# Optimization experiments

Hardware: AMD Instinct MI355X
Metric: run time of the kernel (lower is better)

Reference implementation:

```python
import jax, jax.numpy as jnp
import numpy as np
import math

N_FREQ = 50
ENC_DIM = 4 * N_FREQ  # 200
D = 5
N_GENES = 1000
N_CELLS = 5000
N_FRAG = 200_000


def sine_encoding(coords):
    # frequencies: [f1,f1,f2,f2,...] length 2*N_FREQ; shifts: [0, pi/2, 0, pi/2, ...]
    i = jnp.arange(1, N_FREQ + 1, dtype=jnp.float32)
    freqs = jnp.repeat(1.0 / jnp.power(jnp.float32(1000.0), 2.0 * i / N_FREQ), 2)
    shifts = jnp.tile(jnp.array([0.0, math.pi / 2], jnp.float32), N_FREQ)
    # coords [F,2] -> [F,2,2*nf] -> [F,4*nf]
    return jnp.sin((coords[..., None] * freqs + shifts).reshape(coords.shape[0], -1))


def self_attention(x):
    # x: [G, i, D]; NOTE: scale uses sqrt(seq_len) = sqrt(x.shape[-2]) as in the original
    scores = jnp.einsum('gid,gjd->gij', x, x) / jnp.sqrt(jnp.float32(x.shape[1]))
    w = jax.nn.softmax(scores, axis=-1)
    return jnp.einsum('gij,gjd->gid', w, x)


def setup_inputs() -> dict:
    key = jax.random.key(0)
    ks = jax.random.split(key, 6)
    coordinates = jax.random.uniform(ks[0], (N_FRAG, 2), jnp.float32, -1000.0, 1000.0)
    genemapping = jax.random.randint(ks[1], (N_FRAG,), 0, N_GENES)
    local_cellxgene_ix = jax.random.randint(ks[2], (N_FRAG,), 0, N_CELLS * N_GENES)
    genes_oi = jnp.arange(N_GENES)
    # ragged groups: disjoint fragment index sets for group sizes 2, 3, 4
    n2 = jnp.arange(60000)             # 30000 pairs
    n3 = jnp.arange(60000) + 60000     # 20000 triples
    n4 = jnp.arange(60000) + 120000    # 15000 quads
    stdv = 1.0 / math.sqrt(D)
    weight1_frag = jax.random.uniform(ks[3], (N_GENES, ENC_DIM, D), jnp.float32, -stdv, stdv)
    weight1_expr = jnp.ones((N_GENES, D), jnp.float32)
    bias1 = jax.random.normal(ks[4], (N_GENES,), jnp.float32)  # mean_gene_expression
    return dict(coordinates=coordinates, genemapping=genemapping, n2=n2, n3=n3, n4=n4,
                local_cellxgene_ix=local_cellxgene_ix, genes_oi=genes_oi,
                weight1_frag=weight1_frag, weight1_expr=weight1_expr, bias1=bias1)


def reference(coordinates, genemapping, n2, n3, n4, local_cellxgene_ix, genes_oi,
              weight1_frag, weight1_expr, bias1):
    # FragmentEmbedder: sine encode, per-gene weight gather, contract, sigmoid
    enc = sine_encoding(coordinates)                                 # [F, 200]
    emb = jax.nn.sigmoid(jnp.einsum('fe,fed->fd', enc, weight1_frag[genemapping]))  # [F, 5]
    # ragged self-attention over fixed-size groups (2, 3, 4)
    for idx, i in ((n2, 2), (n3, 3), (n4, 4)):
        x = emb[idx].reshape(-1, i, D)
        emb = emb.at[idx].set(self_attention(x).reshape(-1, D))
    # EmbeddingGenePooler: segment sum over cell x gene
    pooled = jax.ops.segment_sum(emb, local_cellxgene_ix, num_segments=N_CELLS * N_GENES)
    cell_gene_embedding = pooled.reshape(N_CELLS, N_GENES, D)
    # EmbeddingToExpression: gene-wise weighted sum + mean expression bias
    return (cell_gene_embedding * weight1_expr[genes_oi]).sum(-1) + bias1[genes_oi]
```

## Files before the change

### kernel.cpp

```cpp
#include <hip/hip_runtime.h>
#include <math.h>

#define DD 5
#define NFREQ 50
#define NB 128

__global__ __launch_bounds__(256) void blockhist_kernel(
    const int* __restrict__ gm, int F, int chunk,
    int* __restrict__ bc, int n_genes, int* __restrict__ done) {
  __shared__ int cnt[1000];
  if (blockIdx.x == 0 && threadIdx.x == 0) *done = 0;
  for (int j = threadIdx.x; j < n_genes; j += blockDim.x) cnt[j] = 0;
  __syncthreads();
  int b = blockIdx.x;
  int lo = b * chunk;
  int hi = min(F, lo + chunk);
  for (int i = lo + threadIdx.x; i < hi; i += blockDim.x)
    atomicAdd(&cnt[gm[i]], 1);
  __syncthreads();
  for (int j = threadIdx.x; j < n_genes; j += blockDim.x)
    bc[j * NB + b] = cnt[j];
}

__global__ __launch_bounds__(256) void binscan_starts_kernel(
    int* __restrict__ bc, int n_genes, int* __restrict__ totals,
    int* __restrict__ starts, int* __restrict__ done, int nblocks) {
  __shared__ int s_amlast;
  __shared__ int s_ws[4];
  int lane = threadIdx.x & 63;
  int wv = threadIdx.x >> 6;
  int bin = blockIdx.x * 4 + wv;
  if (bin < n_genes) {
    int2* row = (int2*)(bc + (size_t)bin * NB);
    int2 v = row[lane];
    int p = v.x + v.y;
    int ip = p;
#pragma unroll
    for (int off = 1; off < 64; off <<= 1) {
      int q = __shfl_up(ip, off);
      if (lane >= off) ip += q;
    }
    int base = ip - p;
    int2 e;
    e.x = base;
    e.y = base + v.x;
    row[lane] = e;
    if (lane == 63) totals[bin] = ip;
  }
  __syncthreads();
  if (threadIdx.x == 0) {
    __threadfence();
    int tk = atomicAdd(done, 1);
    s_amlast = (tk == nblocks - 1);
  }
  __syncthreads();
  if (!s_amlast) return;
  __threadfence();
  int t = threadIdx.x;
  int4 v = make_int4(0, 0, 0, 0);
  if (4 * t < n_genes) v = ((const int4*)totals)[t];
  int p = v.x + v.y + v.z + v.w;
  int ip = p;
#pragma unroll
  for (int off = 1; off < 64; off <<= 1) {
    int q = __shfl_up(ip, off);
    if (lane >= off) ip += q;
  }
  if (lane == 63) s_ws[wv] = ip;
  __syncthreads();
  int add = 0;
#pragma unroll
  for (int i = 0; i < 4; ++i)
    if (i < wv) add += s_ws[i];
  int excl = add + ip - p;
  int4 e;
  e.x = excl;
  e.y = excl + v.x;
  e.z = e.y + v.y;
  e.w = e.z + v.z;
  if (4 * t < n_genes) ((int4*)starts)[t] = e;
  if (4 * t + 4 == n_genes) starts[n_genes] = e.w + v.w;
}

__global__ __launch_bounds__(256) void blockscatter_kernel(
    const int* __restrict__ gm, int F, int chunk,
    const int* __restrict__ bc, const int* __restrict__ starts,
    int* __restrict__ order, int n_genes) {
  __shared__ int cur[1000];
  int b = blockIdx.x;
  for (int j = threadIdx.x; j < n_genes; j += blockDim.x)
    cur[j] = starts[j] + bc[j * NB + b];
  __syncthreads();
  int lo = b * chunk;
  int hi = min(F, lo + chunk);
  for (int i = lo + threadIdx.x; i < hi; i += blockDim.x) {
    int g = gm[i];
    int p = atomicAdd(&cur[g], 1);
    order[p] = i;
  }
}

__global__ __launch_bounds__(256) void embed_kernel(
    const float2* __restrict__ coords, const int* __restrict__ order,
    const int* __restrict__ starts, const float* __restrict__ W,
    float* __restrict__ emb) {
  __shared__ float s_freq[NFREQ];
  if (threadIdx.x < NFREQ)
    s_freq[threadIdx.x] = exp2f(-0.39863137f * (float)(threadIdx.x + 1));
  __syncthreads();
  int g = blockIdx.x;
  int s0 = starts[g];
  int s1 = starts[g + 1];
  const float* __restrict__ Wg = W + (size_t)g * (4 * NFREQ * DD);

  for (int i = s0 + threadIdx.x; i < s1; i += blockDim.x) {
    int f = order[i];
    float2 xy = coords[f];
    float a0 = 0.f, a1 = 0.f, a2 = 0.f, a3 = 0.f, a4 = 0.f;
    for (int k = 0; k < NFREQ; ++k) {
      float fr = s_freq[k];
      float ax = xy.x * fr;
      float ay = xy.y * fr;
      float sx = __sinf(ax), cx = __cosf(ax);
      float sy = __sinf(ay), cy = __cosf(ay);
      const float* w0s = Wg + (2 * k) * DD;
      const float* w0c = w0s + DD;
      const float* w1s = Wg + (2 * NFREQ + 2 * k) * DD;
      const float* w1c = w1s + DD;
      a0 += sx * w0s[0] + cx * w0c[0] + sy * w1s[0] + cy * w1c[0];
      a1 += sx * w0s[1] + cx * w0c[1] + sy * w1s[1] + cy * w1c[1];
      a2 += sx * w0s[2] + cx * w0c[2] + sy * w1s[2] + cy * w1c[2];
      a3 += sx * w0s[3] + cx * w0c[3] + sy * w1s[3] + cy * w1c[3];
      a4 += sx * w0s[4] + cx * w0c[4] + sy * w1s[4] + cy * w1c[4];
    }
    float* e = emb + (size_t)f * DD;
    e[0] = 1.f / (1.f + __expf(-a0));
    e[1] = 1.f / (1.f + __expf(-a1));
    e[2] = 1.f / (1.f + __expf(-a2));
    e[3] = 1.f / (1.f + __expf(-a3));
    e[4] = 1.f / (1.f + __expf(-a4));
  }
}

template <int SZ>
__device__ __forceinline__ void attn_group(const int* __restrict__ idx,
                                           float* __restrict__ emb) {
  int fid[SZ];
  float x[SZ][DD];
#pragma unroll
  for (int a = 0; a < SZ; ++a) {
    fid[a] = idx[a];
    const float* p = emb + (size_t)fid[a] * DD;
#pragma unroll
    for (int d = 0; d < DD; ++d) x[a][d] = p[d];
  }
  const float scale = rsqrtf((float)SZ);
  float o[SZ][DD];
#pragma unroll
  for (int a = 0; a < SZ; ++a) {
    float sc[SZ];
    float m = -1e30f;
#pragma unroll
    for (int b = 0; b < SZ; ++b) {
      float dt = 0.f;
#pragma unroll
      for (int d = 0; d < DD; ++d) dt += x[a][d] * x[b][d];
      sc[b] = dt * scale;
      m = fmaxf(m, sc[b]);
    }
    float sum = 0.f;
#pragma unroll
    for (int b = 0; b < SZ; ++b) {
      sc[b] = __expf(sc[b] - m);
      sum += sc[b];
    }
    float inv = 1.f / sum;
#pragma unroll
    for (int d = 0; d < DD; ++d) {
      float acc = 0.f;
#pragma unroll
      for (int b = 0; b < SZ; ++b) acc += sc[b] * x[b][d];
      o[a][d] = acc * inv;
    }
  }
#pragma unroll
  for (int a = 0; a < SZ; ++a) {
    float* p = emb + (size_t)fid[a] * DD;
#pragma unroll
    for (int d = 0; d < DD; ++d) p[d] = o[a][d];
  }
}

__global__ __launch_bounds__(256) void attn_init_kernel(
    const int* __restrict__ n2, int g2,
    const int* __restrict__ n3, int g3,
    const int* __restrict__ n4, int g4,
    float* __restrict__ emb, float* __restrict__ out,
    const float* __restrict__ bias, const int* __restrict__ genes_oi,
    int n_genes, int total4) {
  int gtid = blockIdx.x * blockDim.x + threadIdx.x;
  int gs = gridDim.x * blockDim.x;
  int gtot = g2 + g3 + g4;
  for (int w = gtid; w < gtot; w += gs) {
    if (w < g2) attn_group<2>(n2 + (size_t)w * 2, emb);
    else if (w < g2 + g3) attn_group<3>(n3 + (size_t)(w - g2) * 3, emb);
    else attn_group<4>(n4 + (size_t)(w - g2 - g3) * 4, emb);
  }
  for (int v4 = gtid; v4 < total4; v4 += gs) {
    int idx = v4 * 4;
    int j = idx % n_genes;
    float4 vv;
    vv.x = bias[genes_oi[j + 0]];
    vv.y = bias[genes_oi[j + 1]];
    vv.z = bias[genes_oi[j + 2]];
    vv.w = bias[genes_oi[j + 3]];
    reinterpret_cast<float4*>(out)[v4] = vv;
  }
}

__global__ void pool_kernel(const float* __restrict__ emb, const int* __restrict__ lci,
                            const int* __restrict__ genes_oi,
                            const float* __restrict__ wexpr, int F, int n_genes,
                            float* __restrict__ out) {
  int t = blockIdx.x * blockDim.x + threadIdx.x;
  if (t >= F) return;
  int ix = lci[t];
  int gcol = ix % n_genes;
  int g = genes_oi[gcol];
  const float* e = emb + (size_t)t * DD;
  const float* w = wexpr + (size_t)g * DD;
  float s = e[0] * w[0] + e[1] * w[1] + e[2] * w[2] + e[3] * w[3] + e[4] * w[4];
  atomicAdd(out + ix, s);
}

extern "C" void kernel_launch(void* const* d_in, const int* in_sizes, int n_in,
                              void* d_out, int out_size, void* d_ws, size_t ws_size,
                              hipStream_t stream) {
  const float2* coords  = (const float2*)d_in[0];
  const int* gm         = (const int*)d_in[1];
  const int* n2         = (const int*)d_in[2];
  const int* n3         = (const int*)d_in[3];
  const int* n4         = (const int*)d_in[4];
  const int* lci        = (const int*)d_in[5];
  const int* genes_oi   = (const int*)d_in[6];
  const float* W        = (const float*)d_in[7];
  const float* wexpr    = (const float*)d_in[8];
  const float* bias     = (const float*)d_in[9];
  float* out            = (float*)d_out;

  const int F       = in_sizes[1];
  const int n_genes = in_sizes[6];
  const int g2 = in_sizes[2] / 2;
  const int g3 = in_sizes[3] / 3;
  const int g4 = in_sizes[4] / 4;

  char* ws = (char*)d_ws;
  size_t off = 0;
  float* emb   = (float*)(ws + off); off += (size_t)F * DD * sizeof(float);
  int* order   = (int*)(ws + off);   off += (size_t)F * sizeof(int);
  int* bc      = (int*)(ws + off);   off += (size_t)n_genes * NB * sizeof(int);
  off = (off + 15) & ~(size_t)15;
  int* starts  = (int*)(ws + off);   off += (size_t)(n_genes + 4) * sizeof(int);
  off = (off + 15) & ~(size_t)15;
  int* totals  = (int*)(ws + off);   off += (size_t)n_genes * sizeof(int);
  int* done    = (int*)(ws + off);   off += 4 * sizeof(int);

  const int tb = 256;
  const int chunk = (F + NB - 1) / NB;

  blockhist_kernel<<<NB, tb, 0, stream>>>(gm, F, chunk, bc, n_genes, done);
  int scan_blocks = (n_genes + 3) / 4;
  binscan_starts_kernel<<<scan_blocks, tb, 0, stream>>>(bc, n_genes, totals,
                                                        starts, done, scan_blocks);
  blockscatter_kernel<<<NB, tb, 0, stream>>>(gm, F, chunk, bc, starts, order, n_genes);
  embed_kernel<<<n_genes, tb, 0, stream>>>(coords, order, starts, W, emb);
  int total4 = out_size / 4;
  attn_init_kernel<<<1250, tb, 0, stream>>>(n2, g2, n3, g3, n4, g4,
                                            emb, out, bias, genes_oi,
                                            n_genes, total4);
  pool_kernel<<<(F + tb - 1) / tb, tb, 0, stream>>>(emb, lci, genes_oi, wexpr,
                                                    F, n_genes, out);
}
```

Before: 144.5 us.

## Fuse attention with pooling and move output bias init into histogram kernel

The attention step now feeds its outputs straight into the expression dot product and atomic pooling instead of writing emb back and reading it again in a separate pool kernel. A byte mask built during the scan kernel marks fragments that belong to groups, so the fused kernel pools only the ungrouped fragments directly. The bias initialisation of the large output moves into the first histogram kernel, which now runs with more blocks to overlap that fill with the histogram work. This removes one launch and a round trip of emb through memory, at the cost of clearing and scattering the mask and of scattered atomics issued from inside the attention loop.

```diff
diff --git a/kernel.cpp b/kernel.cpp
--- a/kernel.cpp
+++ b/kernel.cpp
@@ -5,28 +5,55 @@
 #define NFREQ 50
 #define NB 128
 
-__global__ __launch_bounds__(256) void blockhist_kernel(
+__global__ __launch_bounds__(256) void hist_init_kernel(
     const int* __restrict__ gm, int F, int chunk,
-    int* __restrict__ bc, int n_genes, int* __restrict__ done) {
+    int* __restrict__ bc, int n_genes, int* __restrict__ done,
+    unsigned char* __restrict__ mask,
+    float* __restrict__ out, const float* __restrict__ bias,
+    const int* __restrict__ genes_oi, int total4) {
   __shared__ int cnt[1000];
-  if (blockIdx.x == 0 && threadIdx.x == 0) *done = 0;
-  for (int j = threadIdx.x; j < n_genes; j += blockDim.x) cnt[j] = 0;
-  __syncthreads();
-  int b = blockIdx.x;
-  int lo = b * chunk;
-  int hi = min(F, lo + chunk);
-  for (int i = lo + threadIdx.x; i < hi; i += blockDim.x)
-    atomicAdd(&cnt[gm[i]], 1);
-  __syncthreads();
-  for (int j = threadIdx.x; j < n_genes; j += blockDim.x)
-    bc[j * NB + b] = cnt[j];
+  const int gtid = blockIdx.x * blockDim.x + threadIdx.x;
+  const int gs = gridDim.x * blockDim.x;
+  if (gtid == 0) *done = 0;
+  int F4 = F >> 2;
+  int* mask4 = (int*)mask;
+  for (int i = gtid; i < F4; i += gs) mask4[i] = 0;
+  for (int i = (F4 << 2) + gtid; i < F; i += gs) mask[i] = 0;
+  for (int v4 = gtid; v4 < total4; v4 += gs) {
+    int idx = v4 * 4;
+    int j = idx % n_genes;
+    float4 vv;
+    vv.x = bias[genes_oi[j + 0]];
+    vv.y = bias[genes_oi[j + 1]];
+    vv.z = bias[genes_oi[j + 2]];
+    vv.w = bias[genes_oi[j + 3]];
+    reinterpret_cast<float4*>(out)[v4] = vv;
+  }
+  if (blockIdx.x < NB) {
+    for (int j = threadIdx.x; j < n_genes; j += blockDim.x) cnt[j] = 0;
+    __syncthreads();
+    int b = blockIdx.x;
+    int lo = b * chunk;
+    int hi = min(F, lo + chunk);
+    for (int i = lo + threadIdx.x; i < hi; i += blockDim.x)
+      atomicAdd(&cnt[gm[i]], 1);
+    __syncthreads();
+    for (int j = threadIdx.x; j < n_genes; j += blockDim.x)
+      bc[j * NB + b] = cnt[j];
+  }
 }
 
 __global__ __launch_bounds__(256) void binscan_starts_kernel(
     int* __restrict__ bc, int n_genes, int* __restrict__ totals,
-    int* __restrict__ starts, int* __restrict__ done, int nblocks) {
+    int* __restrict__ starts, int* __restrict__ done, int nblocks,
+    unsigned char* __restrict__ mask,
+    const int* __restrict__ n2, int c2,
+    const int* __restrict__ n3, int c3,
+    const int* __restrict__ n4, int c4) {
   __shared__ int s_amlast;
   __shared__ int s_ws[4];
+  const int gtid = blockIdx.x * blockDim.x + threadIdx.x;
+  const int gs = gridDim.x * blockDim.x;
   int lane = threadIdx.x & 63;
   int wv = threadIdx.x >> 6;
   int bin = blockIdx.x * 4 + wv;
@@ -47,6 +74,9 @@
     row[lane] = e;
     if (lane == 63) totals[bin] = ip;
   }
+  for (int i = gtid; i < c2; i += gs) mask[n2[i]] = 1;
+  for (int i = gtid; i < c3; i += gs) mask[n3[i]] = 1;
+  for (int i = gtid; i < c4; i += gs) mask[n4[i]] = 1;
   __syncthreads();
   if (threadIdx.x == 0) {
     __threadfence();
@@ -143,8 +173,12 @@
 }
 
 template <int SZ>
-__device__ __forceinline__ void attn_group(const int* __restrict__ idx,
-                                           float* __restrict__ emb) {
+__device__ __forceinline__ void attn_group_pool(const int* __restrict__ idx,
+                                                const float* __restrict__ emb,
+                                                const int* __restrict__ lci,
+                                                const int* __restrict__ genes_oi,
+                                                const float* __restrict__ wexpr,
+                                                int n_genes, float* __restrict__ out) {
   int fid[SZ];
   float x[SZ][DD];
 #pragma unroll
@@ -155,7 +189,6 @@
     for (int d = 0; d < DD; ++d) x[a][d] = p[d];
   }
   const float scale = rsqrtf((float)SZ);
-  float o[SZ][DD];
 #pragma unroll
   for (int a = 0; a < SZ; ++a) {
     float sc[SZ];
@@ -175,62 +208,49 @@
       sum += sc[b];
     }
     float inv = 1.f / sum;
+    int ix = lci[fid[a]];
+    int g = genes_oi[ix % n_genes];
+    const float* w = wexpr + (size_t)g * DD;
+    float s = 0.f;
 #pragma unroll
     for (int d = 0; d < DD; ++d) {
       float acc = 0.f;
 #pragma unroll
       for (int b = 0; b < SZ; ++b) acc += sc[b] * x[b][d];
-      o[a][d] = acc * inv;
-    }
-  }
-#pragma unroll
-  for (int a = 0; a < SZ; ++a) {
-    float* p = emb + (size_t)fid[a] * DD;
-#pragma unroll
-    for (int d = 0; d < DD; ++d) p[d] = o[a][d];
-  }
-}
-
-__global__ __launch_bounds__(256) void attn_init_kernel(
+      s += acc * w[d];
+    }
+    atomicAdd(out + ix, s * inv);
+  }
+}
+
+__global__ __launch_bounds__(256) void attn_pool_kernel(
     const int* __restrict__ n2, int g2,
     const int* __restrict__ n3, int g3,
     const int* __restrict__ n4, int g4,
-    float* __restrict__ emb, float* __restrict__ out,
-    const float* __restrict__ bias, const int* __restrict__ genes_oi,
-    int n_genes, int total4) {
+    const float* __restrict__ emb, const int* __restrict__ lci,
+    const int* __restrict__ genes_oi, const float* __restrict__ wexpr,
+    const unsigned char* __restrict__ mask,
+    int F, int n_genes, float* __restrict__ out) {
   int gtid = blockIdx.x * blockDim.x + threadIdx.x;
   int gs = gridDim.x * blockDim.x;
   int gtot = g2 + g3 + g4;
   for (int w = gtid; w < gtot; w += gs) {
-    if (w < g2) attn_group<2>(n2 + (size_t)w * 2, emb);
-    else if (w < g2 + g3) attn_group<3>(n3 + (size_t)(w - g2) * 3, emb);
-    else attn_group<4>(n4 + (size_t)(w - g2 - g3) * 4, emb);
-  }
-  for (int v4 = gtid; v4 < total4; v4 += gs) {
-    int idx = v4 * 4;
-    int j = idx % n_genes;
-    float4 vv;
-    vv.x = bias[genes_oi[j + 0]];
-    vv.y = bias[genes_oi[j + 1]];
-    vv.z = bias[genes_oi[j + 2]];
-    vv.w = bias[genes_oi[j + 3]];
-    reinterpret_cast<float4*>(out)[v4] = vv;
-  }
-}
-
-__global__ void pool_kernel(const float* __restrict__ emb, const int* __restrict__ lci,
-                            const int* __restrict__ genes_oi,
-                            const float* __restrict__ wexpr, int F, int n_genes,
-                            float* __restrict__ out) {
-  int t = blockIdx.x * blockDim.x + threadIdx.x;
-  if (t >= F) return;
-  int ix = lci[t];
-  int gcol = ix % n_genes;
-  int g = genes_oi[gcol];
-  const float* e = emb + (size_t)t * DD;
-  const float* w = wexpr + (size_t)g * DD;
-  float s = e[0] * w[0] + e[1] * w[1] + e[2] * w[2] + e[3] * w[3] + e[4] * w[4];
-  atomicAdd(out + ix, s);
+    if (w < g2)
+      attn_group_pool<2>(n2 + (size_t)w * 2, emb, lci, genes_oi, wexpr, n_genes, out);
+    else if (w < g2 + g3)
+      attn_group_pool<3>(n3 + (size_t)(w - g2) * 3, emb, lci, genes_oi, wexpr, n_genes, out);
+    else
+      attn_group_pool<4>(n4 + (size_t)(w - g2 - g3) * 4, emb, lci, genes_oi, wexpr, n_genes, out);
+  }
+  for (int f = gtid; f < F; f += gs) {
+    if (mask[f]) continue;
+    int ix = lci[f];
+    int g = genes_oi[ix % n_genes];
+    const float* e = emb + (size_t)f * DD;
+    const float* w = wexpr + (size_t)g * DD;
+    float s = e[0] * w[0] + e[1] * w[1] + e[2] * w[2] + e[3] * w[3] + e[4] * w[4];
+    atomicAdd(out + ix, s);
+  }
 }
 
 extern "C" void kernel_launch(void* const* d_in, const int* in_sizes, int n_in,
@@ -250,9 +270,12 @@
 
   const int F       = in_sizes[1];
   const int n_genes = in_sizes[6];
-  const int g2 = in_sizes[2] / 2;
-  const int g3 = in_sizes[3] / 3;
-  const int g4 = in_sizes[4] / 4;
+  const int c2 = in_sizes[2];
+  const int c3 = in_sizes[3];
+  const int c4 = in_sizes[4];
+  const int g2 = c2 / 2;
+  const int g3 = c3 / 3;
+  const int g4 = c4 / 4;
 
   char* ws = (char*)d_ws;
   size_t off = 0;
@@ -264,20 +287,22 @@
   off = (off + 15) & ~(size_t)15;
   int* totals  = (int*)(ws + off);   off += (size_t)n_genes * sizeof(int);
   int* done    = (int*)(ws + off);   off += 4 * sizeof(int);
+  off = (off + 15) & ~(size_t)15;
+  unsigned char* mask = (unsigned char*)(ws + off); off += (size_t)F;
 
   const int tb = 256;
   const int chunk = (F + NB - 1) / NB;
-
-  blockhist_kernel<<<NB, tb, 0, stream>>>(gm, F, chunk, bc, n_genes, done);
+  const int total4 = out_size / 4;
+
+  hist_init_kernel<<<1024, tb, 0, stream>>>(gm, F, chunk, bc, n_genes, done,
+                                            mask, out, bias, genes_oi, total4);
   int scan_blocks = (n_genes + 3) / 4;
   binscan_starts_kernel<<<scan_blocks, tb, 0, stream>>>(bc, n_genes, totals,
-                                                        starts, done, scan_blocks);
+                                                        starts, done, scan_blocks,
+                                                        mask, n2, c2, n3, c3, n4, c4);
   blockscatter_kernel<<<NB, tb, 0, stream>>>(gm, F, chunk, bc, starts, order, n_genes);
   embed_kernel<<<n_genes, tb, 0, stream>>>(coords, order, starts, W, emb);
-  int total4 = out_size / 4;
-  attn_init_kernel<<<1250, tb, 0, stream>>>(n2, g2, n3, g3, n4, g4,
-                                            emb, out, bias, genes_oi,
-                                            n_genes, total4);
-  pool_kernel<<<(F + tb - 1) / tb, tb, 0, stream>>>(emb, lci, genes_oi, wexpr,
-                                                    F, n_genes, out);
-}
+  attn_pool_kernel<<<1250, tb, 0, stream>>>(n2, g2, n3, g3, n4, g4,
+                                            emb, lci, genes_oi, wexpr,
+                                            mask, F, n_genes, out);
+}
```

New measurement: 142.9 us. No clear change (-1.1%).
